# Optimization experiments

Hardware: AMD Instinct MI355X
Metric: run time of the kernel (lower is better)

Reference implementation:

```python
import jax, jax.numpy as jnp
import numpy as np

# Direction tap offsets (dy, dx) for taps w0, w1, w2 (fix_direction_order=False):
# dir0 horizontal, dir1 vertical, dir2 main diagonal, dir3 anti-diagonal.
DIR_OFFSETS = (
    ((0, -1), (0, 0), (0, 1)),
    ((-1, 0), (0, 0), (1, 0)),
    ((-1, -1), (0, 0), (1, 1)),
    ((1, -1), (0, 0), (-1, 1)),
)

B, CIN, H, W = 1024, 2, 15, 15
M, COUT = 128, 64
N_BLOCKS = 11 // 2 - 1  # 4 DirectionalConvResBlocks


def _shift2d(x, dy, dx):
    # zero-padded shift: out[y, x] = in[y + dy, x + dx]
    if dy == 0 and dx == 0:
        return x
    xp = jnp.pad(x, ((0, 0), (0, 0), (1, 1), (1, 1)))
    h, w = x.shape[-2], x.shape[-1]
    return xp[:, :, 1 + dy:1 + dy + h, 1 + dx:1 + dx + w]


def dir_conv(x, w, b, d):
    # w: [3, Cout, Cin]; true 3-tap line conv along direction d
    offs = DIR_OFFSETS[d]
    y = jnp.einsum('oc,bchw->bohw', w[1], x)
    y = y + jnp.einsum('oc,bchw->bohw', w[0], _shift2d(x, *offs[0]))
    y = y + jnp.einsum('oc,bchw->bohw', w[2], _shift2d(x, *offs[2]))
    return y + b[None, :, None, None]


def conv1x1(x, w, b):
    # w: [Cout, Cin]
    return jnp.einsum('oc,bchw->bohw', w, x) + b[None, :, None, None]


def setup_inputs() -> dict:
    key = jax.random.key(0)
    ks = jax.random.split(key, 16)
    kai_d0 = (2.0 / (3 * CIN)) ** 0.5
    kai_dM = (2.0 / (3 * M)) ** 0.5
    kai_1 = (2.0 / M) ** 0.5
    return {
        'x': jax.random.normal(ks[0], (B, CIN, H, W), jnp.float32),
        'w_d0': jax.random.normal(ks[1], (3, M, CIN), jnp.float32) * kai_d0,
        'b_d0': jnp.zeros((M,), jnp.float32),
        'w_dc': jax.random.normal(ks[2], (N_BLOCKS, 3, M, M), jnp.float32) * kai_dM,
        'b_dc': jnp.zeros((N_BLOCKS, M), jnp.float32),
        'w_px': jax.random.normal(ks[3], (N_BLOCKS, M, M), jnp.float32) * kai_1,
        'b_px': jnp.zeros((N_BLOCKS, M), jnp.float32),
        'w_c1': jax.random.normal(ks[4], (M, M), jnp.float32) * kai_1,
        'b_c1': jnp.zeros((M,), jnp.float32),
        'w_c2': jax.random.normal(ks[5], (M, M), jnp.float32) * kai_1,
        'b_c2': jnp.zeros((M,), jnp.float32),
        'w_f': jax.random.normal(ks[6], (COUT, M), jnp.float32) * kai_1,
        'b_f': jnp.zeros((COUT,), jnp.float32),
    }


def reference(x, w_d0, b_d0, w_dc, b_dc, w_px, b_px, w_c1, b_c1, w_c2, b_c2, w_f, b_f):
    silu = jax.nn.silu
    # initial directional conv + activation (norm='none')
    xs = [silu(dir_conv(x, w_d0, b_d0, d)) for d in range(4)]
    # 4 DirectionalConvResBlocks
    for i in range(N_BLOCKS):
        new = []
        for d in range(4):
            t = silu(dir_conv(xs[d], w_dc[i], b_dc[i], d))
            t = silu(conv1x1(t, w_px[i], b_px[i]))
            new.append(xs[d] + t)
        xs = new
    # Conv0dResBlock (two 1x1 convs, middle_dim_multipler=1)
    xs = [t + silu(conv1x1(silu(conv1x1(t, w_c1, b_c1)), w_c2, b_c2)) for t in xs]
    # final 1x1 conv, stack 4 directions -> [B, 4, Cout, H, W]
    xs = [conv1x1(t, w_f, b_f) for t in xs]
    return jnp.stack(xs, axis=1)
```

## Files before the change

### kernel.cpp

```cpp
#include <hip/hip_runtime.h>

typedef _Float16 half8 __attribute__((ext_vector_type(8)));
typedef _Float16 half4v __attribute__((ext_vector_type(4)));
typedef float float4v __attribute__((ext_vector_type(4)));
typedef float floatx16 __attribute__((ext_vector_type(16)));

#define MFMA16(a,b,c) __builtin_amdgcn_mfma_f32_32x32x16_f16((a),(b),(c),0,0,0)

#define O_D0 0
#define N_D0 768
#define O_DC (O_D0 + N_D0)
#define N_DC 196608
#define O_PX (O_DC + N_DC)
#define N_PX 65536
#define O_C1 (O_PX + N_PX)
#define O_C2 (O_C1 + 16384)
#define O_F  (O_C2 + 16384)
#define W_TOTAL (O_F + 8192)

__global__ void wconv_kernel(const float* __restrict__ w_d0, const float* __restrict__ w_dc,
                             const float* __restrict__ w_px, const float* __restrict__ w_c1,
                             const float* __restrict__ w_c2, const float* __restrict__ w_f,
                             _Float16* __restrict__ ws) {
  int i = blockIdx.x * 256 + threadIdx.x;
  if (i >= W_TOTAL) return;
  float v; int dst;
  if (i < O_DC) {
    v = w_d0[i]; dst = O_D0 + i;
  } else if (i < O_PX) {
    int s = i - O_DC;
    int k = s & 127; int r = s >> 7; int c = r & 127; int bt = r >> 7;
    int t = bt % 3, blk = bt / 3;
    dst = O_DC + blk * 49152 + ((t * 8 + (k >> 4)) * 128 + c) * 16 + (k & 15);
    v = w_dc[s];
  } else if (i < O_C1) {
    int s = i - O_PX;
    int k = s & 127; int r = s >> 7; int c = r & 127; int blk = r >> 7;
    dst = O_PX + blk * 16384 + ((k >> 4) * 128 + c) * 16 + (k & 15);
    v = w_px[s];
  } else if (i < O_C2) {
    int s = i - O_C1;
    int k = s & 127; int c = s >> 7;
    dst = O_C1 + ((k >> 4) * 128 + c) * 16 + (k & 15);
    v = w_c1[s];
  } else if (i < O_F) {
    int s = i - O_C2;
    int k = s & 127; int c = s >> 7;
    dst = O_C2 + ((k >> 4) * 128 + c) * 16 + (k & 15);
    v = w_c2[s];
  } else {
    int s = i - O_F;
    int k = s & 127; int c = s >> 7;
    dst = O_F + ((k >> 4) * 64 + c) * 16 + (k & 15);
    v = w_f[s];
  }
  ws[dst] = (_Float16)v;
}

__device__ __forceinline__ float silu_f(float v) {
  float e = __expf(-v);
  return v * __builtin_amdgcn_rcpf(1.0f + e);
}

__device__ __forceinline__ floatx16 bias_init(const float* biasL, int slot, int cbase) {
  floatx16 a;
  const float* bp = biasL + slot * 128 + cbase;
#pragma unroll
  for (int g = 0; g < 4; ++g) {
    float4v v = *(const float4v*)(bp + 8 * g);
    a[4*g+0] = v[0]; a[4*g+1] = v[1]; a[4*g+2] = v[2]; a[4*g+3] = v[3];
  }
  return a;
}

template<int KSTRIDE>
__device__ __forceinline__ void gemm_pass(
    const _Float16* asrc, int row0,
    const _Float16* __restrict__ wq,
    int boff, int lk8, floatx16 acc[2])
{
  const int pb0 = row0 * 128;
  const int psw = (row0 & 15) << 3;
#pragma unroll
  for (int kk = 0; kk < 8; ++kk) {
    const int kx = (kk * 16 + lk8) ^ psw;
    half8 a  = *(const half8*)&asrc[pb0 + kx];
    half8 w0 = *(const half8*)&wq[kk * KSTRIDE + boff];
    half8 w1 = *(const half8*)&wq[kk * KSTRIDE + boff + 512];
    acc[0] = MFMA16(w0, a, acc[0]);
    acc[1] = MFMA16(w1, a, acc[1]);
  }
}

__device__ __forceinline__ void store_silu(_Float16* dst, int p, int cbase, const floatx16& a) {
  const int base = p * 128, s = (p & 15) << 3;
#pragma unroll
  for (int g = 0; g < 4; ++g) {
    half4v h;
#pragma unroll
    for (int j = 0; j < 4; ++j) h[j] = (_Float16)silu_f(a[4*g+j]);
    *(half4v*)&dst[base + ((cbase + 8*g) ^ s)] = h;
  }
}

__device__ __forceinline__ void store_silu_masked(_Float16* Abp, int pa, int cbase,
                                                  const floatx16& a, bool valid) {
  if (!valid) return;
  const int base = pa * 128, s = (pa & 15) << 3;
#pragma unroll
  for (int g = 0; g < 4; ++g) {
    half4v h;
#pragma unroll
    for (int j = 0; j < 4; ++j) h[j] = (_Float16)silu_f(a[4*g+j]);
    *(half4v*)&Abp[base + ((cbase + 8*g) ^ s)] = h;
  }
}

__device__ __forceinline__ void resid_update(_Float16* Abp, int pa, int cbase,
                                             const floatx16& a, bool valid) {
  if (!valid) return;
  const int base = pa * 128, s = (pa & 15) << 3;
#pragma unroll
  for (int g = 0; g < 4; ++g) {
    int off = base + ((cbase + 8*g) ^ s);
    half4v r = *(const half4v*)&Abp[off];
    half4v h;
#pragma unroll
    for (int j = 0; j < 4; ++j) h[j] = (_Float16)((float)r[j] + silu_f(a[4*g+j]));
    *(half4v*)&Abp[off] = h;
  }
}

__global__ __launch_bounds__(1024, 1) void mixnet_kernel(
    const float* __restrict__ xin, const _Float16* __restrict__ ws,
    const float* __restrict__ b_d0, const float* __restrict__ b_dc,
    const float* __restrict__ b_px, const float* __restrict__ b_c1,
    const float* __restrict__ b_c2, const float* __restrict__ b_f,
    float* __restrict__ out)
{
  __shared__ _Float16 Ab[290 * 128];
  __shared__ _Float16 Bb[256 * 128];
  __shared__ float biasL[12 * 128];

  const int bid = blockIdx.x;
  const int b = bid >> 2, d = bid & 3;
  const int tid = threadIdx.x;
  const int wv = tid >> 6, l = tid & 63;
  const int mg = wv >> 1, ng = wv & 1;
  const int lrow = l & 31;
  const int lk8 = (l >> 5) << 3;
  const int lhalf = l >> 5;

  static const int DYT[4][3] = {{0,0,0},{-1,0,1},{-1,0,1},{1,0,-1}};
  static const int DXT[4][3] = {{-1,0,1},{0,0,0},{-1,0,1},{-1,0,1}};
  const int sh0 = DYT[d][0] * 16 + DXT[d][0];
  const int sh2 = DYT[d][2] * 16 + DXT[d][2];

  const int p0 = mg * 32 + lrow;
  const int boff = (ng * 64 + lrow) * 16 + lk8;
  const int cb0 = ng * 64 + 4 * lhalf;
  const int cb1 = cb0 + 32;
  const bool v0 = (p0 >= 16) && (p0 < 255) && ((p0 & 15) < 15);

  {
    int* Ai = (int*)Ab;
    for (int i = tid; i < 290 * 128 / 2; i += 1024) Ai[i] = 0;
  }
  for (int i = tid; i < 12 * 128; i += 1024) {
    int slot = i >> 7, c = i & 127; float v;
    if (slot == 0)       v = b_d0[c];
    else if (slot < 5)   v = b_dc[(slot - 1) * 128 + c];
    else if (slot < 9)   v = b_px[(slot - 5) * 128 + c];
    else if (slot == 9)  v = b_c1[c];
    else if (slot == 10) v = b_c2[c];
    else                 v = (c < 64) ? b_f[c] : 0.0f;
    biasL[i] = v;
  }
  _Float16* Axt = Bb;
  _Float16* wBs = Bb + 4096;
  {
    int* Bi = (int*)Bb;
    for (int i = tid; i < (4096 + 2048) / 2; i += 1024) Bi[i] = 0;
  }
  __syncthreads();
  for (int i = tid; i < 256 * 8; i += 1024) {
    int f = i >> 3, k = i & 7;
    if (k < 6) {
      int t = k >> 1, ci = k & 1;
      int y = (f >> 4) - 1 + DYT[d][t];
      int xx = (f & 15) + DXT[d][t];
      float v = 0.0f;
      if (y >= 0 && y < 15 && xx >= 0 && xx < 15)
        v = xin[b * 450 + ci * 225 + y * 15 + xx];
      Axt[f * 16 + k] = (_Float16)v;
    }
  }
  for (int i = tid; i < 128 * 8; i += 1024) {
    int c = i >> 3, k = i & 7;
    if (k < 6) {
      int t = k >> 1, ci = k & 1;
      wBs[c * 16 + k] = ws[O_D0 + (t * 128 + c) * 2 + ci];
    }
  }
  __syncthreads();

  {
    half8 a  = *(const half8*)&Axt[p0 * 16 + lk8];
    half8 w0 = *(const half8*)&wBs[(ng * 64 + lrow) * 16 + lk8];
    half8 w1 = *(const half8*)&wBs[(ng * 64 + 32 + lrow) * 16 + lk8];
    floatx16 acc0 = bias_init(biasL, 0, cb0);
    floatx16 acc1 = bias_init(biasL, 0, cb1);
    acc0 = MFMA16(w0, a, acc0);
    acc1 = MFMA16(w1, a, acc1);
    __syncthreads();
    store_silu_masked(Ab, p0 + 17, cb0, acc0, v0);
    store_silu_masked(Ab, p0 + 17, cb1, acc1, v0);
  }
  __syncthreads();

  floatx16 acc[2];
  const _Float16* wdc = ws + O_DC;
  const _Float16* wpx = ws + O_PX;

#pragma unroll 1
  for (int blk = 0; blk < 4; ++blk) {
    {
      const _Float16* wt = wdc + blk * 49152;
      acc[0] = bias_init(biasL, 1 + blk, cb0);
      acc[1] = bias_init(biasL, 1 + blk, cb1);
      gemm_pass<2048>(Ab, 17 + p0 + sh0, wt,         boff, lk8, acc);
      gemm_pass<2048>(Ab, 17 + p0,       wt + 16384, boff, lk8, acc);
      gemm_pass<2048>(Ab, 17 + p0 + sh2, wt + 32768, boff, lk8, acc);
      store_silu(Bb, p0, cb0, acc[0]);
      store_silu(Bb, p0, cb1, acc[1]);
    }
    __syncthreads();
    {
      acc[0] = bias_init(biasL, 5 + blk, cb0);
      acc[1] = bias_init(biasL, 5 + blk, cb1);
      gemm_pass<2048>(Bb, p0, wpx + blk * 16384, boff, lk8, acc);
      resid_update(Ab, p0 + 17, cb0, acc[0], v0);
      resid_update(Ab, p0 + 17, cb1, acc[1], v0);
    }
    __syncthreads();
  }

  {
    acc[0] = bias_init(biasL, 9, cb0);
    acc[1] = bias_init(biasL, 9, cb1);
    gemm_pass<2048>(Ab, 17 + p0, ws + O_C1, boff, lk8, acc);
    store_silu(Bb, p0, cb0, acc[0]);
    store_silu(Bb, p0, cb1, acc[1]);
  }
  __syncthreads();
  {
    acc[0] = bias_init(biasL, 10, cb0);
    acc[1] = bias_init(biasL, 10, cb1);
    gemm_pass<2048>(Bb, p0, ws + O_C2, boff, lk8, acc);
    resid_update(Ab, p0 + 17, cb0, acc[0], v0);
    resid_update(Ab, p0 + 17, cb1, acc[1], v0);
  }
  __syncthreads();

  if (ng == 0) {
    acc[0] = bias_init(biasL, 11, 4 * lhalf);
    acc[1] = bias_init(biasL, 11, 32 + 4 * lhalf);
    gemm_pass<1024>(Ab, 17 + p0, ws + O_F, lrow * 16 + lk8, lk8, acc);
  }
  __syncthreads();
  float* stg = (float*)Bb;
  if (ng == 0 && v0) {
    int y = (p0 >> 4) - 1, xx = p0 & 15;
    int pix = y * 15 + xx;
#pragma unroll
    for (int nn = 0; nn < 2; ++nn) {
      int cb = nn * 32 + 4 * lhalf;
#pragma unroll
      for (int j = 0; j < 16; ++j) {
        int c = cb + (j & 3) + 8 * (j >> 2);
        stg[c * 225 + pix] = acc[nn][j];
      }
    }
  }
  __syncthreads();
  {
    size_t base = (size_t)bid * 14400;
    for (int i = tid; i < 14400; i += 1024)
      __builtin_nontemporal_store(stg[i], &out[base + i]);
  }
}

extern "C" void kernel_launch(void* const* d_in, const int* in_sizes, int n_in,
                              void* d_out, int out_size, void* d_ws, size_t ws_size,
                              hipStream_t stream) {
  (void)in_sizes; (void)n_in; (void)out_size;
  const float* x    = (const float*)d_in[0];
  const float* w_d0 = (const float*)d_in[1];
  const float* b_d0 = (const float*)d_in[2];
  const float* w_dc = (const float*)d_in[3];
  const float* b_dc = (const float*)d_in[4];
  const float* w_px = (const float*)d_in[5];
  const float* b_px = (const float*)d_in[6];
  const float* w_c1 = (const float*)d_in[7];
  const float* b_c1 = (const float*)d_in[8];
  const float* w_c2 = (const float*)d_in[9];
  const float* b_c2 = (const float*)d_in[10];
  const float* w_f  = (const float*)d_in[11];
  const float* b_f  = (const float*)d_in[12];
  float* out = (float*)d_out;
  _Float16* ws = (_Float16*)d_ws;
  if (ws_size < (size_t)W_TOTAL * sizeof(_Float16)) return;

  wconv_kernel<<<(W_TOTAL + 255) / 256, 256, 0, stream>>>(w_d0, w_dc, w_px, w_c1, w_c2, w_f, ws);
  mixnet_kernel<<<4096, 1024, 0, stream>>>(x, ws, b_d0, b_dc, b_px, b_c1, b_c2, b_f, out);
}
```

Measured before the change: 990.1 us.

## Register-block two pixel tiles per wave to reuse weight fragments, halve block size

Each wave now computes two 32-row pixel tiles instead of one, so every weight fragment loaded from global memory feeds four MFMAs instead of two. The block shrinks from 1024 to 512 threads, and all strided loops and the launch configuration are adjusted to match. This targets the repeated global and L2 weight traffic in the inner GEMM loops. The cost is doubled accumulator registers per wave and half as many waves to hide latency, since shared-memory usage still limits residency to about one block per CU.

```diff
diff --git a/kernel.cpp b/kernel.cpp
--- a/kernel.cpp
+++ b/kernel.cpp
@@ -77,18 +77,21 @@
 __device__ __forceinline__ void gemm_pass(
     const _Float16* asrc, int row0,
     const _Float16* __restrict__ wq,
-    int boff, int lk8, floatx16 acc[2])
+    int boff, int lk8, floatx16 acc[2][2])
 {
   const int pb0 = row0 * 128;
   const int psw = (row0 & 15) << 3;
 #pragma unroll
   for (int kk = 0; kk < 8; ++kk) {
     const int kx = (kk * 16 + lk8) ^ psw;
-    half8 a  = *(const half8*)&asrc[pb0 + kx];
+    half8 a0 = *(const half8*)&asrc[pb0 + kx];
+    half8 a1 = *(const half8*)&asrc[pb0 + 4096 + kx];
     half8 w0 = *(const half8*)&wq[kk * KSTRIDE + boff];
     half8 w1 = *(const half8*)&wq[kk * KSTRIDE + boff + 512];
-    acc[0] = MFMA16(w0, a, acc[0]);
-    acc[1] = MFMA16(w1, a, acc[1]);
+    acc[0][0] = MFMA16(w0, a0, acc[0][0]);
+    acc[0][1] = MFMA16(w1, a0, acc[0][1]);
+    acc[1][0] = MFMA16(w0, a1, acc[1][0]);
+    acc[1][1] = MFMA16(w1, a1, acc[1][1]);
   }
 }
 
@@ -131,7 +134,7 @@
   }
 }
 
-__global__ __launch_bounds__(1024, 1) void mixnet_kernel(
+__global__ __launch_bounds__(512, 2) void mixnet_kernel(
     const float* __restrict__ xin, const _Float16* __restrict__ ws,
     const float* __restrict__ b_d0, const float* __restrict__ b_dc,
     const float* __restrict__ b_px, const float* __restrict__ b_c1,
@@ -156,17 +159,19 @@
   const int sh0 = DYT[d][0] * 16 + DXT[d][0];
   const int sh2 = DYT[d][2] * 16 + DXT[d][2];
 
-  const int p0 = mg * 32 + lrow;
+  const int p0 = mg * 64 + lrow;
+  const int p1 = p0 + 32;
   const int boff = (ng * 64 + lrow) * 16 + lk8;
   const int cb0 = ng * 64 + 4 * lhalf;
   const int cb1 = cb0 + 32;
   const bool v0 = (p0 >= 16) && (p0 < 255) && ((p0 & 15) < 15);
+  const bool v1 = (p1 >= 16) && (p1 < 255) && ((p1 & 15) < 15);
 
   {
     int* Ai = (int*)Ab;
-    for (int i = tid; i < 290 * 128 / 2; i += 1024) Ai[i] = 0;
-  }
-  for (int i = tid; i < 12 * 128; i += 1024) {
+    for (int i = tid; i < 290 * 128 / 2; i += 512) Ai[i] = 0;
+  }
+  for (int i = tid; i < 12 * 128; i += 512) {
     int slot = i >> 7, c = i & 127; float v;
     if (slot == 0)       v = b_d0[c];
     else if (slot < 5)   v = b_dc[(slot - 1) * 128 + c];
@@ -180,10 +185,10 @@
   _Float16* wBs = Bb + 4096;
   {
     int* Bi = (int*)Bb;
-    for (int i = tid; i < (4096 + 2048) / 2; i += 1024) Bi[i] = 0;
-  }
-  __syncthreads();
-  for (int i = tid; i < 256 * 8; i += 1024) {
+    for (int i = tid; i < (4096 + 2048) / 2; i += 512) Bi[i] = 0;
+  }
+  __syncthreads();
+  for (int i = tid; i < 256 * 8; i += 512) {
     int f = i >> 3, k = i & 7;
     if (k < 6) {
       int t = k >> 1, ci = k & 1;
@@ -195,7 +200,7 @@
       Axt[f * 16 + k] = (_Float16)v;
     }
   }
-  for (int i = tid; i < 128 * 8; i += 1024) {
+  for (int i = tid; i < 128 * 8; i += 512) {
     int c = i >> 3, k = i & 7;
     if (k < 6) {
       int t = k >> 1, ci = k & 1;
@@ -205,20 +210,26 @@
   __syncthreads();
 
   {
-    half8 a  = *(const half8*)&Axt[p0 * 16 + lk8];
+    half8 a0 = *(const half8*)&Axt[p0 * 16 + lk8];
+    half8 a1 = *(const half8*)&Axt[p1 * 16 + lk8];
     half8 w0 = *(const half8*)&wBs[(ng * 64 + lrow) * 16 + lk8];
     half8 w1 = *(const half8*)&wBs[(ng * 64 + 32 + lrow) * 16 + lk8];
-    floatx16 acc0 = bias_init(biasL, 0, cb0);
-    floatx16 acc1 = bias_init(biasL, 0, cb1);
-    acc0 = MFMA16(w0, a, acc0);
-    acc1 = MFMA16(w1, a, acc1);
+    floatx16 a00 = bias_init(biasL, 0, cb0);
+    floatx16 a01 = bias_init(biasL, 0, cb1);
+    floatx16 a10 = a00, a11 = a01;
+    a00 = MFMA16(w0, a0, a00);
+    a01 = MFMA16(w1, a0, a01);
+    a10 = MFMA16(w0, a1, a10);
+    a11 = MFMA16(w1, a1, a11);
     __syncthreads();
-    store_silu_masked(Ab, p0 + 17, cb0, acc0, v0);
-    store_silu_masked(Ab, p0 + 17, cb1, acc1, v0);
-  }
-  __syncthreads();
-
-  floatx16 acc[2];
+    store_silu_masked(Ab, p0 + 17, cb0, a00, v0);
+    store_silu_masked(Ab, p0 + 17, cb1, a01, v0);
+    store_silu_masked(Ab, p1 + 17, cb0, a10, v1);
+    store_silu_masked(Ab, p1 + 17, cb1, a11, v1);
+  }
+  __syncthreads();
+
+  floatx16 acc[2][2];
   const _Float16* wdc = ws + O_DC;
   const _Float16* wpx = ws + O_PX;
 
@@ -226,66 +237,91 @@
   for (int blk = 0; blk < 4; ++blk) {
     {
       const _Float16* wt = wdc + blk * 49152;
-      acc[0] = bias_init(biasL, 1 + blk, cb0);
-      acc[1] = bias_init(biasL, 1 + blk, cb1);
+      acc[0][0] = bias_init(biasL, 1 + blk, cb0);
+      acc[0][1] = bias_init(biasL, 1 + blk, cb1);
+      acc[1][0] = acc[0][0];
+      acc[1][1] = acc[0][1];
       gemm_pass<2048>(Ab, 17 + p0 + sh0, wt,         boff, lk8, acc);
       gemm_pass<2048>(Ab, 17 + p0,       wt + 16384, boff, lk8, acc);
       gemm_pass<2048>(Ab, 17 + p0 + sh2, wt + 32768, boff, lk8, acc);
-      store_silu(Bb, p0, cb0, acc[0]);
-      store_silu(Bb, p0, cb1, acc[1]);
+      store_silu(Bb, p0, cb0, acc[0][0]);
+      store_silu(Bb, p0, cb1, acc[0][1]);
+      store_silu(Bb, p1, cb0, acc[1][0]);
+      store_silu(Bb, p1, cb1, acc[1][1]);
     }
     __syncthreads();
     {
-      acc[0] = bias_init(biasL, 5 + blk, cb0);
-      acc[1] = bias_init(biasL, 5 + blk, cb1);
+      acc[0][0] = bias_init(biasL, 5 + blk, cb0);
+      acc[0][1] = bias_init(biasL, 5 + blk, cb1);
+      acc[1][0] = acc[0][0];
+      acc[1][1] = acc[0][1];
       gemm_pass<2048>(Bb, p0, wpx + blk * 16384, boff, lk8, acc);
-      resid_update(Ab, p0 + 17, cb0, acc[0], v0);
-      resid_update(Ab, p0 + 17, cb1, acc[1], v0);
+      resid_update(Ab, p0 + 17, cb0, acc[0][0], v0);
+      resid_update(Ab, p0 + 17, cb1, acc[0][1], v0);
+      resid_update(Ab, p1 + 17, cb0, acc[1][0], v1);
+      resid_update(Ab, p1 + 17, cb1, acc[1][1], v1);
     }
     __syncthreads();
   }
 
   {
-    acc[0] = bias_init(biasL, 9, cb0);
-    acc[1] = bias_init(biasL, 9, cb1);
+    acc[0][0] = bias_init(biasL, 9, cb0);
+    acc[0][1] = bias_init(biasL, 9, cb1);
+    acc[1][0] = acc[0][0];
+    acc[1][1] = acc[0][1];
     gemm_pass<2048>(Ab, 17 + p0, ws + O_C1, boff, lk8, acc);
-    store_silu(Bb, p0, cb0, acc[0]);
-    store_silu(Bb, p0, cb1, acc[1]);
-  }
-  __syncthreads();
-  {
-    acc[0] = bias_init(biasL, 10, cb0);
-    acc[1] = bias_init(biasL, 10, cb1);
+    store_silu(Bb, p0, cb0, acc[0][0]);
+    store_silu(Bb, p0, cb1, acc[0][1]);
+    store_silu(Bb, p1, cb0, acc[1][0]);
+    store_silu(Bb, p1, cb1, acc[1][1]);
+  }
+  __syncthreads();
+  {
+    acc[0][0] = bias_init(biasL, 10, cb0);
+    acc[0][1] = bias_init(biasL, 10, cb1);
+    acc[1][0] = acc[0][0];
+    acc[1][1] = acc[0][1];
     gemm_pass<2048>(Bb, p0, ws + O_C2, boff, lk8, acc);
-    resid_update(Ab, p0 + 17, cb0, acc[0], v0);
-    resid_update(Ab, p0 + 17, cb1, acc[1], v0);
+    resid_update(Ab, p0 + 17, cb0, acc[0][0], v0);
+    resid_update(Ab, p0 + 17, cb1, acc[0][1], v0);
+    resid_update(Ab, p1 + 17, cb0, acc[1][0], v1);
+    resid_update(Ab, p1 + 17, cb1, acc[1][1], v1);
   }
   __syncthreads();
 
   if (ng == 0) {
-    acc[0] = bias_init(biasL, 11, 4 * lhalf);
-    acc[1] = bias_init(biasL, 11, 32 + 4 * lhalf);
+    acc[0][0] = bias_init(biasL, 11, 4 * lhalf);
+    acc[0][1] = bias_init(biasL, 11, 32 + 4 * lhalf);
+    acc[1][0] = acc[0][0];
+    acc[1][1] = acc[0][1];
     gemm_pass<1024>(Ab, 17 + p0, ws + O_F, lrow * 16 + lk8, lk8, acc);
   }
   __syncthreads();
   float* stg = (float*)Bb;
-  if (ng == 0 && v0) {
-    int y = (p0 >> 4) - 1, xx = p0 & 15;
-    int pix = y * 15 + xx;
-#pragma unroll
-    for (int nn = 0; nn < 2; ++nn) {
-      int cb = nn * 32 + 4 * lhalf;
-#pragma unroll
-      for (int j = 0; j < 16; ++j) {
-        int c = cb + (j & 3) + 8 * (j >> 2);
-        stg[c * 225 + pix] = acc[nn][j];
+  if (ng == 0) {
+#pragma unroll
+    for (int mm = 0; mm < 2; ++mm) {
+      int p = p0 + mm * 32;
+      bool vm = mm ? v1 : v0;
+      if (vm) {
+        int y = (p >> 4) - 1, xx = p & 15;
+        int pix = y * 15 + xx;
+#pragma unroll
+        for (int nn = 0; nn < 2; ++nn) {
+          int cb = nn * 32 + 4 * lhalf;
+#pragma unroll
+          for (int j = 0; j < 16; ++j) {
+            int c = cb + (j & 3) + 8 * (j >> 2);
+            stg[c * 225 + pix] = acc[mm][nn][j];
+          }
+        }
       }
     }
   }
   __syncthreads();
   {
     size_t base = (size_t)bid * 14400;
-    for (int i = tid; i < 14400; i += 1024)
+    for (int i = tid; i < 14400; i += 512)
       __builtin_nontemporal_store(stg[i], &out[base + i]);
   }
 }
@@ -312,5 +348,5 @@
   if (ws_size < (size_t)W_TOTAL * sizeof(_Float16)) return;
 
   wconv_kernel<<<(W_TOTAL + 255) / 256, 256, 0, stream>>>(w_d0, w_dc, w_px, w_c1, w_c2, w_f, ws);
-  mixnet_kernel<<<4096, 1024, 0, stream>>>(x, ws, b_d0, b_dc, b_px, b_c1, b_c2, b_f, out);
-}
+  mixnet_kernel<<<4096, 512, 0, stream>>>(x, ws, b_d0, b_dc, b_px, b_c1, b_c2, b_f, out);
+}
```

Measured after the change: 1.013 ms. +2.3%, slower.
